# Kernel optimization log

Measured on AMD Instinct MI355X. Metric: run time of the kernel, lower is better.

Reference implementation:

```python
import jax, jax.numpy as jnp
import numpy as np

INPUT_SIZE = 28
HIDDEN = 64
TIME_STEP = 28
OUT_DIM = 10


def setup_inputs() -> dict:
    key = jax.random.key(0)
    ks = jax.random.split(key, 7)
    B = 32768
    s_ih = 1.0 / np.sqrt(HIDDEN)
    X = jax.random.normal(ks[0], (B, TIME_STEP, INPUT_SIZE), dtype=jnp.float32)
    W_ih = jax.random.uniform(ks[1], (HIDDEN, INPUT_SIZE), jnp.float32, -s_ih, s_ih)
    W_hh = jax.random.uniform(ks[2], (HIDDEN, HIDDEN), jnp.float32, -s_ih, s_ih)
    b_ih = jax.random.uniform(ks[3], (HIDDEN,), jnp.float32, -s_ih, s_ih)
    b_hh = jax.random.uniform(ks[4], (HIDDEN,), jnp.float32, -s_ih, s_ih)
    s_o = 1.0 / np.sqrt(HIDDEN)
    W_out = jax.random.uniform(ks[5], (OUT_DIM, HIDDEN), jnp.float32, -s_o, s_o)
    b_out = jax.random.uniform(ks[6], (OUT_DIM,), jnp.float32, -s_o, s_o)
    return {"X": X, "W_ih": W_ih, "W_hh": W_hh, "b_ih": b_ih, "b_hh": b_hh,
            "W_out": W_out, "b_out": b_out}


def reference(X, W_ih, W_hh, b_ih, b_hh, W_out, b_out):
    B = X.shape[0]
    # Precompute input projections for all steps in one GEMM: [B,T,H]
    x_proj = jnp.einsum('bti,hi->bth', X, W_ih) + b_ih + b_hh

    def step(h, xp):
        # h: [B,H], xp: [B,H]
        h_new = jnp.tanh(xp + h @ W_hh.T)
        return h_new, None

    h0 = jnp.zeros((B, HIDDEN), dtype=X.dtype)
    h_last, _ = jax.lax.scan(step, h0, jnp.swapaxes(x_proj, 0, 1))
    # Final linear on last hidden state (== h_state of last layer)
    return h_last @ W_out.T + b_out
```

## Files before the change

### kernel.cpp

```cpp
#include <hip/hip_runtime.h>

#define TT 28
#define II 28
#define HH 64
#define OO 10

typedef __attribute__((ext_vector_type(8))) __bf16 bf16x8;
typedef __attribute__((ext_vector_type(4))) float f32x4;

union FragU { unsigned u[4]; bf16x8 v; };

__device__ __forceinline__ unsigned short f2bf(float f) {
    unsigned u = __builtin_bit_cast(unsigned, f);
    return (unsigned short)((u + 0x7FFFu + ((u >> 16) & 1u)) >> 16);
}
__device__ __forceinline__ float bf2f(unsigned short s) {
    return __builtin_bit_cast(float, (unsigned)s << 16);
}
__device__ __forceinline__ unsigned pk(float lo, float hi) {
    return (unsigned)f2bf(lo) | ((unsigned)f2bf(hi) << 16);
}

#define MFMA(A, B, C) __builtin_amdgcn_mfma_f32_16x16x32_bf16((A), (B), (C), 0, 0, 0)

__global__ __launch_bounds__(256, 2) void rnn_mfma(
    const float* __restrict__ X, const float* __restrict__ W_ih,
    const float* __restrict__ W_hh, const float* __restrict__ b_ih,
    const float* __restrict__ b_hh, const float* __restrict__ W_out,
    const float* __restrict__ b_out, float* __restrict__ out)
{
    const int lane = threadIdx.x & 63;
    const int wave = threadIdx.x >> 6;
    const int m15  = lane & 15;
    const int g    = lane >> 4;
    const bool hiHalf = (g >> 1) != 0;
    const int bglob = blockIdx.x * 64 + wave * 16 + m15;

    FragU whhhi[4][2], whhlo[4][2];
    #pragma unroll
    for (int jt = 0; jt < 4; ++jt) {
        #pragma unroll
        for (int kb = 0; kb < 2; ++kb) {
            const float* p = W_hh + (16 * jt + m15) * HH + 32 * kb + 8 * g;
            float4 a = *(const float4*)p;
            float4 c = *(const float4*)(p + 4);
            float w[8] = {a.x, a.y, a.z, a.w, c.x, c.y, c.z, c.w};
            #pragma unroll
            for (int u = 0; u < 4; ++u) {
                unsigned hw = pk(w[2 * u], w[2 * u + 1]);
                whhhi[jt][kb].u[u] = hw;
                whhlo[jt][kb].u[u] =
                    pk(w[2 * u]     - bf2f((unsigned short)(hw & 0xFFFFu)),
                       w[2 * u + 1] - bf2f((unsigned short)(hw >> 16)));
            }
        }
    }

    FragU wihhi[4], wihlo[4];
    #pragma unroll
    for (int jt = 0; jt < 4; ++jt) {
        int j = 16 * jt + m15;
        float wv[8];
        #pragma unroll
        for (int e = 0; e < 8; ++e) {
            int k = 8 * g + e;
            float v = 0.f;
            if (k < II)       v = W_ih[j * II + k];
            else if (k == II) v = b_ih[j] + b_hh[j];
            wv[e] = v;
        }
        #pragma unroll
        for (int u = 0; u < 4; ++u) {
            unsigned hw = pk(wv[2 * u], wv[2 * u + 1]);
            wihhi[jt].u[u] = hw;
            wihlo[jt].u[u] =
                pk(wv[2 * u]     - bf2f((unsigned short)(hw & 0xFFFFu)),
                   wv[2 * u + 1] - bf2f((unsigned short)(hw >> 16)));
        }
    }

    int idx[4];
    #pragma unroll
    for (int w = 0; w < 4; ++w)
        idx[w] = 4 * (m15 + 16 * (2 * (g & 1) + (w >> 1)));

    const float* xbase = X + (size_t)bglob * (TT * II);

    float4 xr0, xr1;
    {
        const float* p = xbase + 8 * g;
        xr0 = *(const float4*)p;
        xr1 = (g < 3) ? *(const float4*)(p + 4) : make_float4(1.f, 0.f, 0.f, 0.f);
    }

    FragU hhi[2], hlo[2];
    float th[4][4];

    for (int t = 0; t < TT; ++t) {
        float xv[8] = {xr0.x, xr0.y, xr0.z, xr0.w, xr1.x, xr1.y, xr1.z, xr1.w};
        FragU xhi, xlo;
        #pragma unroll
        for (int u = 0; u < 4; ++u) {
            unsigned hw = pk(xv[2 * u], xv[2 * u + 1]);
            xhi.u[u] = hw;
            xlo.u[u] = pk(xv[2 * u]     - bf2f((unsigned short)(hw & 0xFFFFu)),
                          xv[2 * u + 1] - bf2f((unsigned short)(hw >> 16)));
        }
        if (t < TT - 1) {
            const float* p = xbase + (t + 1) * II + 8 * g;
            xr0 = *(const float4*)p;
            xr1 = (g < 3) ? *(const float4*)(p + 4) : make_float4(1.f, 0.f, 0.f, 0.f);
        }

        f32x4 accv[4];
        #pragma unroll
        for (int jt = 0; jt < 4; ++jt) {
            f32x4 a = {0.f, 0.f, 0.f, 0.f};
            a = MFMA(wihhi[jt].v, xhi.v, a);
            a = MFMA(wihhi[jt].v, xlo.v, a);
            a = MFMA(wihlo[jt].v, xhi.v, a);
            accv[jt] = a;
        }
        if (t > 0) {
            #pragma unroll
            for (int jt = 0; jt < 4; ++jt) {
                f32x4 a = accv[jt];
                #pragma unroll
                for (int kb = 0; kb < 2; ++kb) {
                    a = MFMA(whhhi[jt][kb].v, hhi[kb].v, a);
                    a = MFMA(whhhi[jt][kb].v, hlo[kb].v, a);
                    a = MFMA(whhlo[jt][kb].v, hhi[kb].v, a);
                }
                accv[jt] = a;
            }
        }

        #pragma unroll
        for (int jt = 0; jt < 4; ++jt) {
            #pragma unroll
            for (int r = 0; r < 4; ++r) {
                float aa = accv[jt][r];
                float e = __expf(2.f * aa);
                th[jt][r] = 1.f - 2.f * __builtin_amdgcn_rcpf(e + 1.f);
            }
        }

        if (t < TT - 1) {
            unsigned phi[4][2], plo[4][2];
            #pragma unroll
            for (int jt = 0; jt < 4; ++jt) {
                #pragma unroll
                for (int u = 0; u < 2; ++u) {
                    unsigned hw = pk(th[jt][2 * u], th[jt][2 * u + 1]);
                    phi[jt][u] = hw;
                    plo[jt][u] =
                        pk(th[jt][2 * u]     - bf2f((unsigned short)(hw & 0xFFFFu)),
                           th[jt][2 * u + 1] - bf2f((unsigned short)(hw >> 16)));
                }
            }
            #pragma unroll
            for (int kb = 0; kb < 2; ++kb) {
                #pragma unroll
                for (int w = 0; w < 4; ++w) {
                    int c0 = __builtin_amdgcn_ds_bpermute(idx[w], (int)phi[2 * kb][w & 1]);
                    int c1 = __builtin_amdgcn_ds_bpermute(idx[w], (int)phi[2 * kb + 1][w & 1]);
                    hhi[kb].u[w] = (unsigned)(hiHalf ? c1 : c0);
                    c0 = __builtin_amdgcn_ds_bpermute(idx[w], (int)plo[2 * kb][w & 1]);
                    c1 = __builtin_amdgcn_ds_bpermute(idx[w], (int)plo[2 * kb + 1][w & 1]);
                    hlo[kb].u[w] = (unsigned)(hiHalf ? c1 : c0);
                }
            }
        }
    }

    float po[OO];
    #pragma unroll
    for (int o = 0; o < OO; ++o) {
        float s = 0.f;
        #pragma unroll
        for (int jt = 0; jt < 4; ++jt) {
            float4 wv = *(const float4*)(W_out + o * HH + 16 * jt + 4 * g);
            s += th[jt][0] * wv.x + th[jt][1] * wv.y +
                 th[jt][2] * wv.z + th[jt][3] * wv.w;
        }
        s += __shfl_xor(s, 16);
        s += __shfl_xor(s, 32);
        po[o] = s;
    }
    if (g == 0) {
        #pragma unroll
        for (int o = 0; o < OO; ++o)
            out[(size_t)bglob * OO + o] = po[o] + b_out[o];
    }
}

extern "C" void kernel_launch(void* const* d_in, const int* in_sizes, int n_in,
                              void* d_out, int out_size, void* d_ws, size_t ws_size,
                              hipStream_t stream) {
    const float* X     = (const float*)d_in[0];
    const float* W_ih  = (const float*)d_in[1];
    const float* W_hh  = (const float*)d_in[2];
    const float* b_ih  = (const float*)d_in[3];
    const float* b_hh  = (const float*)d_in[4];
    const float* W_out = (const float*)d_in[5];
    const float* b_out = (const float*)d_in[6];
    float* out = (float*)d_out;

    const int B = in_sizes[0] / (TT * II);
    dim3 grid(B / 64), block(256);
    hipLaunchKernelGGL(rnn_mfma, grid, block, 0, stream,
                       X, W_ih, W_hh, b_ih, b_hh, W_out, b_out, out);
}
```

Before: 64.53 us.

## Permute hidden-unit rows so MFMA output feeds next step without bpermute

Reorders the hidden-unit rows assigned to each MFMA output tile so that each lane's accumulator outputs already sit in the B-operand layout needed for the next recurrent step. This removes the 16 ds_bpermute cross-lane shuffles and selects per timestep on the serial critical path. It also swaps the manual bf16 round-to-nearest bit arithmetic for native bf16 conversion casts, which can lower to packed hardware conversion instructions. The W_out indexing is adjusted to match the new row permutation, and any mismatch in the mapping would give wrong results.

Result: faster. 52.99 us, median of 2 (-17.9%).

```diff
diff --git a/kernel.cpp b/kernel.cpp
--- a/kernel.cpp
+++ b/kernel.cpp
@@ -6,24 +6,26 @@
 #define OO 10
 
 typedef __attribute__((ext_vector_type(8))) __bf16 bf16x8;
+typedef __attribute__((ext_vector_type(2))) __bf16 bf16x2;
 typedef __attribute__((ext_vector_type(4))) float f32x4;
 
 union FragU { unsigned u[4]; bf16x8 v; };
 
-__device__ __forceinline__ unsigned short f2bf(float f) {
-    unsigned u = __builtin_bit_cast(unsigned, f);
-    return (unsigned short)((u + 0x7FFFu + ((u >> 16) & 1u)) >> 16);
+__device__ __forceinline__ unsigned cvtpk(float f0, float f1) {
+    bf16x2 p; p.x = (__bf16)f0; p.y = (__bf16)f1;
+    return __builtin_bit_cast(unsigned, p);
 }
-__device__ __forceinline__ float bf2f(unsigned short s) {
-    return __builtin_bit_cast(float, (unsigned)s << 16);
-}
-__device__ __forceinline__ unsigned pk(float lo, float hi) {
-    return (unsigned)f2bf(lo) | ((unsigned)f2bf(hi) << 16);
+__device__ __forceinline__ void split2(float f0, float f1, unsigned& hi, unsigned& lo) {
+    unsigned hb = cvtpk(f0, f1);
+    float h0 = __builtin_bit_cast(float, hb << 16);
+    float h1 = __builtin_bit_cast(float, hb & 0xFFFF0000u);
+    lo = cvtpk(f0 - h0, f1 - h1);
+    hi = hb;
 }
 
 #define MFMA(A, B, C) __builtin_amdgcn_mfma_f32_16x16x32_bf16((A), (B), (C), 0, 0, 0)
 
-__global__ __launch_bounds__(256, 2) void rnn_mfma(
+__global__ __launch_bounds__(256, 2) void rnn_mfma2(
     const float* __restrict__ X, const float* __restrict__ W_ih,
     const float* __restrict__ W_hh, const float* __restrict__ b_ih,
     const float* __restrict__ b_hh, const float* __restrict__ W_out,
@@ -33,56 +35,43 @@
     const int wave = threadIdx.x >> 6;
     const int m15  = lane & 15;
     const int g    = lane >> 4;
-    const bool hiHalf = (g >> 1) != 0;
     const int bglob = blockIdx.x * 64 + wave * 16 + m15;
+    const int rowhi = 8 * (m15 >> 2) + (m15 & 3);
 
     FragU whhhi[4][2], whhlo[4][2];
     #pragma unroll
     for (int jt = 0; jt < 4; ++jt) {
+        const int jA = 32 * (jt >> 1) + 4 * (jt & 1) + rowhi;
         #pragma unroll
         for (int kb = 0; kb < 2; ++kb) {
-            const float* p = W_hh + (16 * jt + m15) * HH + 32 * kb + 8 * g;
+            const float* p = W_hh + jA * HH + 32 * kb + 8 * g;
             float4 a = *(const float4*)p;
             float4 c = *(const float4*)(p + 4);
             float w[8] = {a.x, a.y, a.z, a.w, c.x, c.y, c.z, c.w};
             #pragma unroll
-            for (int u = 0; u < 4; ++u) {
-                unsigned hw = pk(w[2 * u], w[2 * u + 1]);
-                whhhi[jt][kb].u[u] = hw;
-                whhlo[jt][kb].u[u] =
-                    pk(w[2 * u]     - bf2f((unsigned short)(hw & 0xFFFFu)),
-                       w[2 * u + 1] - bf2f((unsigned short)(hw >> 16)));
-            }
+            for (int u = 0; u < 4; ++u)
+                split2(w[2 * u], w[2 * u + 1],
+                       whhhi[jt][kb].u[u], whhlo[jt][kb].u[u]);
         }
     }
 
     FragU wihhi[4], wihlo[4];
     #pragma unroll
     for (int jt = 0; jt < 4; ++jt) {
-        int j = 16 * jt + m15;
+        const int jA = 32 * (jt >> 1) + 4 * (jt & 1) + rowhi;
         float wv[8];
         #pragma unroll
         for (int e = 0; e < 8; ++e) {
             int k = 8 * g + e;
             float v = 0.f;
-            if (k < II)       v = W_ih[j * II + k];
-            else if (k == II) v = b_ih[j] + b_hh[j];
+            if (k < II)       v = W_ih[jA * II + k];
+            else if (k == II) v = b_ih[jA] + b_hh[jA];
             wv[e] = v;
         }
         #pragma unroll
-        for (int u = 0; u < 4; ++u) {
-            unsigned hw = pk(wv[2 * u], wv[2 * u + 1]);
-            wihhi[jt].u[u] = hw;
-            wihlo[jt].u[u] =
-                pk(wv[2 * u]     - bf2f((unsigned short)(hw & 0xFFFFu)),
-                   wv[2 * u + 1] - bf2f((unsigned short)(hw >> 16)));
-        }
+        for (int u = 0; u < 4; ++u)
+            split2(wv[2 * u], wv[2 * u + 1], wihhi[jt].u[u], wihlo[jt].u[u]);
     }
-
-    int idx[4];
-    #pragma unroll
-    for (int w = 0; w < 4; ++w)
-        idx[w] = 4 * (m15 + 16 * (2 * (g & 1) + (w >> 1)));
 
     const float* xbase = X + (size_t)bglob * (TT * II);
 
@@ -100,12 +89,9 @@
         float xv[8] = {xr0.x, xr0.y, xr0.z, xr0.w, xr1.x, xr1.y, xr1.z, xr1.w};
         FragU xhi, xlo;
         #pragma unroll
-        for (int u = 0; u < 4; ++u) {
-            unsigned hw = pk(xv[2 * u], xv[2 * u + 1]);
-            xhi.u[u] = hw;
-            xlo.u[u] = pk(xv[2 * u]     - bf2f((unsigned short)(hw & 0xFFFFu)),
-                          xv[2 * u + 1] - bf2f((unsigned short)(hw >> 16)));
-        }
+        for (int u = 0; u < 4; ++u)
+            split2(xv[2 * u], xv[2 * u + 1], xhi.u[u], xlo.u[u]);
+
         if (t < TT - 1) {
             const float* p = xbase + (t + 1) * II + 8 * g;
             xr0 = *(const float4*)p;
@@ -146,29 +132,23 @@
         }
 
         if (t < TT - 1) {
-            unsigned phi[4][2], plo[4][2];
+            unsigned thh[4][2], thl[4][2];
             #pragma unroll
-            for (int jt = 0; jt < 4; ++jt) {
+            for (int jt = 0; jt < 4; ++jt)
                 #pragma unroll
-                for (int u = 0; u < 2; ++u) {
-                    unsigned hw = pk(th[jt][2 * u], th[jt][2 * u + 1]);
-                    phi[jt][u] = hw;
-                    plo[jt][u] =
-                        pk(th[jt][2 * u]     - bf2f((unsigned short)(hw & 0xFFFFu)),
-                           th[jt][2 * u + 1] - bf2f((unsigned short)(hw >> 16)));
-                }
-            }
+                for (int u = 0; u < 2; ++u)
+                    split2(th[jt][2 * u], th[jt][2 * u + 1],
+                           thh[jt][u], thl[jt][u]);
             #pragma unroll
             for (int kb = 0; kb < 2; ++kb) {
-                #pragma unroll
-                for (int w = 0; w < 4; ++w) {
-                    int c0 = __builtin_amdgcn_ds_bpermute(idx[w], (int)phi[2 * kb][w & 1]);
-                    int c1 = __builtin_amdgcn_ds_bpermute(idx[w], (int)phi[2 * kb + 1][w & 1]);
-                    hhi[kb].u[w] = (unsigned)(hiHalf ? c1 : c0);
-                    c0 = __builtin_amdgcn_ds_bpermute(idx[w], (int)plo[2 * kb][w & 1]);
-                    c1 = __builtin_amdgcn_ds_bpermute(idx[w], (int)plo[2 * kb + 1][w & 1]);
-                    hlo[kb].u[w] = (unsigned)(hiHalf ? c1 : c0);
-                }
+                hhi[kb].u[0] = thh[2 * kb][0];
+                hhi[kb].u[1] = thh[2 * kb][1];
+                hhi[kb].u[2] = thh[2 * kb + 1][0];
+                hhi[kb].u[3] = thh[2 * kb + 1][1];
+                hlo[kb].u[0] = thl[2 * kb][0];
+                hlo[kb].u[1] = thl[2 * kb][1];
+                hlo[kb].u[2] = thl[2 * kb + 1][0];
+                hlo[kb].u[3] = thl[2 * kb + 1][1];
             }
         }
     }
@@ -179,7 +159,8 @@
         float s = 0.f;
         #pragma unroll
         for (int jt = 0; jt < 4; ++jt) {
-            float4 wv = *(const float4*)(W_out + o * HH + 16 * jt + 4 * g);
+            const float* wp = W_out + o * HH + 32 * (jt >> 1) + 8 * g + 4 * (jt & 1);
+            float4 wv = *(const float4*)wp;
             s += th[jt][0] * wv.x + th[jt][1] * wv.y +
                  th[jt][2] * wv.z + th[jt][3] * wv.w;
         }
@@ -208,6 +189,6 @@
 
     const int B = in_sizes[0] / (TT * II);
     dim3 grid(B / 64), block(256);
-    hipLaunchKernelGGL(rnn_mfma, grid, block, 0, stream,
+    hipLaunchKernelGGL(rnn_mfma2, grid, block, 0, stream,
                        X, W_ih, W_hh, b_ih, b_hh, W_out, b_out, out);
 }
```
